# Kernel optimization log

Hardware: AMD Instinct MI355X
Metric: run time of the kernel (lower is better)

## Reference

```python
import jax, jax.numpy as jnp
import numpy as np

# dims
B, S, A = 16384, 300, 30
EMB, M_TOK, M_PROTO = 256, 8, 16
H_ENC, H_DEC, MF, NZ = 256, 128, 12, 4
ALPHA_MIN, ALPHA_MAX, ETA0 = 0.06, 0.3, 0.1
TECH_IDX = jnp.array([61, 91, 121, 151, 181, 211, 241, 271])


def setup_inputs() -> dict:
    key = jax.random.key(0)
    ks = jax.random.split(key, 20)
    def w(k, shape, fan):
        return jax.random.normal(k, shape, jnp.float32) * (fan ** -0.5)
    return {
        'state':   jax.random.uniform(ks[0], (B, S), jnp.float32),
        'fitness': jax.random.uniform(ks[1], (B, M_PROTO), jnp.float32),
        'proto_keys': jax.random.normal(ks[2], (M_PROTO, EMB), jnp.float32) * (EMB ** -0.5),
        'enc_W1': w(ks[3], (S, H_ENC), S),   'enc_b1': jnp.zeros((H_ENC,), jnp.float32),
        'ln_g':   jnp.ones((H_ENC,), jnp.float32), 'ln_b': jnp.zeros((H_ENC,), jnp.float32),
        'enc_W2': w(ks[4], (H_ENC, M_TOK * EMB), H_ENC), 'enc_b2': jnp.zeros((M_TOK * EMB,), jnp.float32),
        'dec_W1': w(ks[5], (M_PROTO, EMB, H_DEC), EMB),  'dec_b1': jnp.zeros((M_PROTO, H_DEC), jnp.float32),
        'dec_W2': w(ks[6], (M_PROTO, H_DEC, A), H_DEC),  'dec_b2': jnp.zeros((M_PROTO, A), jnp.float32),
        'tc_W':  w(ks[7], (MF, EMB), MF),  'tc_b':  jnp.zeros((EMB,), jnp.float32),
        'tc_cW': w(ks[8], (EMB, 1), EMB),  'tc_cb': jnp.zeros((1,), jnp.float32),
        'tc_zW': w(ks[9], (EMB, NZ), EMB), 'tc_zb': jnp.zeros((NZ,), jnp.float32),
        'w_prev': jnp.full((1, M_PROTO), 1.0 / M_PROTO, jnp.float32),
    }


def _layernorm(x, g, b, eps=1e-5):
    mu = x.mean(-1, keepdims=True)
    var = ((x - mu) ** 2).mean(-1, keepdims=True)
    return (x - mu) * jax.lax.rsqrt(var + eps) * g + b


def _forward(state, fitness, proto_keys, enc_W1, enc_b1, ln_g, ln_b, enc_W2, enc_b2,
             dec_W1, dec_b1, dec_W2, dec_b2, tc_W, tc_b, tc_cW, tc_cb, tc_zW, tc_zb, w_prev):
    # --- market feature extraction ---
    balance = state[:, 0:1]
    prices = state[:, 1:31]
    shares = state[:, 31:61]
    price_mean = prices.mean(1, keepdims=True)
    price_std = jnp.std(prices, axis=1, keepdims=True, ddof=1) + 1e-8  # torch.std is unbiased
    total_value = balance + (prices * shares).sum(1, keepdims=True)
    cash_ratio = balance / (total_value + 1e-8)
    tech = state[:, TECH_IDX]
    mf = jnp.concatenate([balance, price_mean, price_std, cash_ratio, tech], axis=1)  # [B,12]
    # --- T-Cell (minimal surrogate: danger embed, crisis level, crisis types) ---
    danger = jnp.tanh(mf @ tc_W + tc_b)                     # [B,EMB]
    crisis = jax.nn.sigmoid(danger @ tc_cW + tc_cb)         # [B,1]
    z = jax.nn.softmax(danger @ tc_zW + tc_zb, axis=-1)     # [B,NZ]
    # --- epitope encoder: Linear -> LN -> ReLU -> Linear -> reshape [B,m,EMB] ---
    h = jax.nn.relu(_layernorm(state @ enc_W1 + enc_b1, ln_g, ln_b))
    E = (h @ enc_W2 + enc_b2).reshape(-1, M_TOK, EMB)
    # --- IRT routing (OT-attention + fitness replicator, crisis-gated mix) ---
    scale = EMB ** -0.5
    logits = jnp.einsum('bme,ne->bmn', E, proto_keys) * scale \
           + (jnp.einsum('be,ne->bn', danger, proto_keys) * scale)[:, None, :]  # [B,m,M]
    P = jax.nn.softmax(logits, axis=-1)
    w_ot = P.mean(axis=1)                                   # [B,M]
    w_rep = w_prev * jnp.exp(ETA0 * fitness)
    w_rep = w_rep / (w_rep.sum(-1, keepdims=True) + 1e-8)
    alpha_c = ALPHA_MIN + (ALPHA_MAX - ALPHA_MIN) * (1.0 - crisis)  # [B,1]
    w = alpha_c * w_ot + (1.0 - alpha_c) * w_rep
    w = w / (w.sum(-1, keepdims=True) + 1e-8)
    # --- per-expert decoders on proto_keys (batched GEMM over M experts) ---
    hd = jax.nn.relu(jnp.einsum('me,meh->mh', proto_keys, dec_W1) + dec_b1)
    conc = jax.nn.softplus(jnp.einsum('mh,mha->ma', hd, dec_W2) + dec_b2)  # [M,A]
    mixed = jnp.einsum('bm,ma->ba', w, conc) + 1.0          # [B,A]
    # deterministic branch: softmax action head
    action = jax.nn.softmax(mixed, axis=-1)
    action = jnp.clip(action, 0.0, 1.0)
    action = action / (action.sum(-1, keepdims=True) + 1e-8)
    return action


def reference(state, fitness, proto_keys, enc_W1, enc_b1, ln_g, ln_b, enc_W2, enc_b2,
              dec_W1, dec_b1, dec_W2, dec_b2, tc_W, tc_b, tc_cW, tc_cb, tc_zW, tc_zb, w_prev):
    return _forward(state, fitness, proto_keys, enc_W1, enc_b1, ln_g, ln_b, enc_W2, enc_b2,
                    dec_W1, dec_b1, dec_W2, dec_b2, tc_W, tc_b, tc_cW, tc_cb, tc_zW, tc_zb, w_prev)
```

## Files before the change

kernel.cpp:

```cpp
#include <hip/hip_runtime.h>

typedef __attribute__((ext_vector_type(8))) short bf16x8;
typedef __attribute__((ext_vector_type(4))) float f32x4;

#define NBATCH 16384
#define SS     300
#define AA     30
#define ROWS   16
#define SSTR   352
#define HSTR   280
#define LSTR   132
#define K1P    320
#define SCALEF 0.0625f
#define ETA0   0.1f

__device__ __forceinline__ short f2b(float x) {
    unsigned u = __float_as_uint(x);
    unsigned r = (u + 0x7FFFu + ((u >> 16) & 1u)) >> 16;
    return (short)r;
}
__device__ __forceinline__ float b2f(short s) {
    return __uint_as_float(((unsigned)(unsigned short)s) << 16);
}
__device__ __forceinline__ float tanh_fast(float x) {
    float e = __expf(2.f * x);
    return 1.f - 2.f / (e + 1.f);
}

__global__ __launch_bounds__(256) void pre_kernel(
    const float* __restrict__ proto, const float* __restrict__ W1,
    const float* __restrict__ W2,   const float* __restrict__ b2,
    const float* __restrict__ tcW,  const float* __restrict__ cW,
    const float* __restrict__ dW1,  const float* __restrict__ db1,
    const float* __restrict__ dW2,  const float* __restrict__ db2,
    short* __restrict__ W1P, short* __restrict__ W3P,
    short* __restrict__ PDP, short* __restrict__ TCP,
    float* __restrict__ cmn, float* __restrict__ conc)
{
    __shared__ short sbuf[64 * 264 + 4096];
    const int t = threadIdx.x;
    const int bid = blockIdx.x;

    if (bid < 32) {
        const int m = bid >> 2, jt = bid & 3;
        short* W2s = sbuf;
        short* prS = sbuf + 64 * 264;
        #pragma unroll 4
        for (int it = 0; it < 64; ++it) {
            const int idx = it * 256 + t, j = idx >> 8, e = idx & 255;
            W2s[j * 264 + e] = f2b(W2[(size_t)(jt * 64 + j) * 2048 + m * 256 + e]);
        }
        for (int it = 0; it < 16; ++it) {
            const int id = it * 256 + t, chunk = id >> 3, j8 = id & 7;
            const int kt = chunk >> 6, rem = chunk & 63, q = rem >> 4, n = rem & 15;
            prS[id] = f2b(proto[n * 256 + kt * 32 + q * 8 + j8]);
        }
        __syncthreads();
        const int lane = t & 63, wv = t >> 6, l15 = lane & 15, q = lane >> 4;
        f32x4 acc = {0.f, 0.f, 0.f, 0.f};
        for (int kt = 0; kt < 8; ++kt) {
            bf16x8 a = *(const bf16x8*)&W2s[(wv * 16 + l15) * 264 + kt * 32 + q * 8];
            bf16x8 b = *(const bf16x8*)&prS[((kt * 4 + q) * 16 + l15) * 8];
            acc = __builtin_amdgcn_mfma_f32_16x16x32_bf16(a, b, acc, 0, 0, 0);
        }
        #pragma unroll
        for (int reg = 0; reg < 4; ++reg) {
            const int jg = jt * 64 + wv * 16 + q * 4 + reg;
            const int c = m * 16 + l15;
            const int ktj = jg >> 5, qj = (jg >> 3) & 3, j8 = jg & 7;
            W3P[((ktj * 4 + qj) * 128 + c) * 8 + j8] = f2b(acc[reg]);
        }
    } else if (bid < 42) {
        const int kt = bid - 32;
        short* W1s = sbuf;
        #pragma unroll 4
        for (int it = 0; it < 32; ++it) {
            const int idx = it * 256 + t, k = idx >> 8, n = idx & 255;
            const int kg = kt * 32 + k;
            W1s[k * 256 + n] = (kg < SS) ? f2b(W1[(size_t)kg * 256 + n]) : (short)0;
        }
        __syncthreads();
        for (int it = 0; it < 4; ++it) {
            const int id = it * 256 + t, q = id >> 8, n = id & 255;
            bf16x8 v;
            #pragma unroll
            for (int j = 0; j < 8; ++j) v[j] = W1s[(q * 8 + j) * 256 + n];
            *(bf16x8*)&W1P[((kt * 4 + q) * 256 + n) * 8] = v;
        }
    } else if (bid == 42) {
        for (int it = 0; it < 32; ++it) {
            const int id = it * 256 + t, chunk = id >> 3, j8 = id & 7;
            const int kt = chunk >> 7, q = (chunk >> 5) & 3, np = chunk & 31;
            const int k = kt * 32 + q * 8 + j8;
            float v = 0.f;
            if (np < 16) v = proto[np * 256 + k];
            else if (np == 16) v = cW[k];
            PDP[id] = f2b(v);
        }
    } else if (bid == 43) {
        for (int it = 0; it < 32; ++it) {
            const int id = it * 256 + t, chunk = id >> 3, j8 = id & 7;
            const int q = chunk >> 8, n = chunk & 255, k = q * 8 + j8;
            TCP[id] = (k < 12) ? f2b(tcW[k * 256 + n]) : (short)0;
        }
    } else if (bid == 44) {
        float* b2s = (float*)sbuf;
        float* prF = (float*)sbuf + 2048;
        for (int it = 0; it < 8; ++it)  b2s[it * 256 + t] = b2[it * 256 + t];
        for (int it = 0; it < 16; ++it) prF[it * 256 + t] = proto[it * 256 + t];
        __syncthreads();
        if (t < 128) {
            const int mq = t >> 4, n = t & 15;
            float acc = 0.f;
            for (int e = 0; e < 256; ++e) acc += b2s[mq * 256 + e] * prF[n * 256 + e];
            cmn[t] = acc;
        }
    } else {
        const int m = bid - 45;
        float* hd = (float*)sbuf;
        if (t < 128) {
            float acc = db1[m * 128 + t];
            const float* wp = dW1 + (size_t)m * 256 * 128 + t;
            const float* p = proto + m * 256;
            for (int e = 0; e < 256; ++e) acc += p[e] * wp[e * 128];
            hd[t] = fmaxf(acc, 0.f);
        }
        __syncthreads();
        if (t < AA) {
            float acc = db2[m * AA + t];
            const float* wp = dW2 + (size_t)m * 128 * AA + t;
            for (int h = 0; h < 128; ++h) acc += hd[h] * wp[h * AA];
            conc[m * AA + t] = fmaxf(acc, 0.f) + log1pf(__expf(-fabsf(acc)));
        }
    }
}

__global__ __launch_bounds__(256, 5) void main_kernel(
    const float* __restrict__ state, const float* __restrict__ fitness,
    const float* __restrict__ b1,
    const float* __restrict__ lng,  const float* __restrict__ lnb,
    const float* __restrict__ tcb,  const float* __restrict__ cb,
    const float* __restrict__ pw,
    const short* __restrict__ W1P,  const short* __restrict__ W3P,
    const short* __restrict__ PDP,  const short* __restrict__ TCP,
    const float* __restrict__ cmn,  const float* __restrict__ conc,
    float* __restrict__ out)
{
    const int t    = threadIdx.x;
    const int row0 = blockIdx.x * ROWS;
    const int w    = t >> 6;
    const int lane = t & 63;
    const int l15  = lane & 15;
    const int q    = lane >> 4;

    __shared__ short sA[ROWS * SSTR];
    __shared__ short sB[ROWS * HSTR];
    __shared__ short s_mfB[ROWS * 32];
    __shared__ float s_red[ROWS][8];
    __shared__ float s_mu[ROWS], s_rstd[ROWS];
    __shared__ float s_dd[ROWS * 16];
    __shared__ float s_crisis[ROWS];
    __shared__ float s_cmn[128];
    __shared__ float s_conc[16 * AA];

    float* s_log  = (float*)sB;
    float* s_wrep = (float*)&sA[ROWS * HSTR];

    #pragma unroll 4
    for (int it = 0; it < 20; ++it) {
        const int idx = it * 256 + t, r = idx / K1P, k = idx - r * K1P;
        sA[r * SSTR + k] = (k < SS) ? f2b(state[(size_t)(row0 + r) * SS + k]) : (short)0;
    }
    for (int it = t; it < 128 + 16 * AA; it += 256) {
        if (it < 128) s_cmn[it] = cmn[it];
        else s_conc[it - 128] = conc[it - 128];
    }
    __syncthreads();

    {
        const int r = t >> 4, g = t & 15;
        float sp = 0.f, sp2 = 0.f, sps = 0.f;
        if (g < 15) {
            #pragma unroll
            for (int jj = 0; jj < 2; ++jj) {
                const int i = 2 * g + jj;
                const float p = b2f(sA[r * SSTR + 1 + i]);
                const float s = b2f(sA[r * SSTR + 31 + i]);
                sp += p; sp2 += p * p; sps += p * s;
            }
        }
        #pragma unroll
        for (int off = 1; off < 16; off <<= 1) {
            sp  += __shfl_xor(sp, off);
            sp2 += __shfl_xor(sp2, off);
            sps += __shfl_xor(sps, off);
        }
        if (g < 8) s_mfB[r * 32 + 4 + g] = sA[r * SSTR + 61 + 30 * g];
        for (int k = 12 + g; k < 32; k += 16) s_mfB[r * 32 + k] = 0;
        if (g == 0) {
            const float bal = b2f(sA[r * SSTR]);
            const float pm = sp * (1.f / 30.f);
            const float var = (sp2 - 30.f * pm * pm) * (1.f / 29.f);
            const float pstd = sqrtf(fmaxf(var, 0.f)) + 1e-8f;
            s_mfB[r * 32 + 0] = sA[r * SSTR];
            s_mfB[r * 32 + 1] = f2b(pm);
            s_mfB[r * 32 + 2] = f2b(pstd);
            s_mfB[r * 32 + 3] = f2b(bal / (bal + sps + 1e-8f));
        }
    }
    __syncthreads();

    {
        f32x4 dacc[4];
        #pragma unroll
        for (int u = 0; u < 4; ++u) dacc[u] = (f32x4){0.f, 0.f, 0.f, 0.f};
        bf16x8 a = *(const bf16x8*)&s_mfB[l15 * 32 + q * 8];
        #pragma unroll
        for (int u = 0; u < 4; ++u) {
            bf16x8 b = *(const bf16x8*)&TCP[((q << 8) | (w * 64 + u * 16 + l15)) * 8];
            dacc[u] = __builtin_amdgcn_mfma_f32_16x16x32_bf16(a, b, dacc[u], 0, 0, 0);
        }
        #pragma unroll
        for (int u = 0; u < 4; ++u) {
            const int col = w * 64 + u * 16 + l15;
            const float tb = tcb[col];
            #pragma unroll
            for (int reg = 0; reg < 4; ++reg)
                sB[(q * 4 + reg) * HSTR + col] = f2b(tanh_fast(dacc[u][reg] + tb));
        }
    }
    __syncthreads();

    if (w == 0) {
        f32x4 acc = {0.f, 0.f, 0.f, 0.f};
        for (int kt = 0; kt < 8; ++kt) {
            bf16x8 a = *(const bf16x8*)&sB[l15 * HSTR + kt * 32 + q * 8];
            bf16x8 b = *(const bf16x8*)&PDP[((kt * 4 + q) * 32 + l15) * 8];
            acc = __builtin_amdgcn_mfma_f32_16x16x32_bf16(a, b, acc, 0, 0, 0);
        }
        #pragma unroll
        for (int reg = 0; reg < 4; ++reg)
            s_dd[(q * 4 + reg) * 16 + l15] = acc[reg];
    } else if (w == 1) {
        f32x4 acc = {0.f, 0.f, 0.f, 0.f};
        for (int kt = 0; kt < 8; ++kt) {
            bf16x8 a = *(const bf16x8*)&sB[l15 * HSTR + kt * 32 + q * 8];
            bf16x8 b = *(const bf16x8*)&PDP[((kt * 4 + q) * 32 + 16 + l15) * 8];
            acc = __builtin_amdgcn_mfma_f32_16x16x32_bf16(a, b, acc, 0, 0, 0);
        }
        if (l15 == 0) {
            const float cbv = cb[0];
            #pragma unroll
            for (int reg = 0; reg < 4; ++reg)
                s_crisis[q * 4 + reg] = 1.f / (1.f + __expf(-(acc[reg] + cbv)));
        }
    }

    f32x4 acc[4];
    #pragma unroll
    for (int u = 0; u < 4; ++u) acc[u] = (f32x4){0.f, 0.f, 0.f, 0.f};
    for (int kt = 0; kt < 10; ++kt) {
        bf16x8 a = *(const bf16x8*)&sA[l15 * SSTR + kt * 32 + q * 8];
        bf16x8 bfr[4];
        #pragma unroll
        for (int u = 0; u < 4; ++u)
            bfr[u] = *(const bf16x8*)&W1P[((kt * 4 + q) * 256 + (w * 64 + u * 16 + l15)) * 8];
        #pragma unroll
        for (int u = 0; u < 4; ++u)
            acc[u] = __builtin_amdgcn_mfma_f32_16x16x32_bf16(a, bfr[u], acc[u], 0, 0, 0);
    }

    {
        float b1v[4];
        #pragma unroll
        for (int u = 0; u < 4; ++u) b1v[u] = b1[w * 64 + u * 16 + l15];
        #pragma unroll
        for (int reg = 0; reg < 4; ++reg) {
            float s = 0.f, s2 = 0.f;
            #pragma unroll
            for (int u = 0; u < 4; ++u) {
                const float v = acc[u][reg] + b1v[u];
                acc[u][reg] = v;
                s += v; s2 += v * v;
            }
            #pragma unroll
            for (int off = 1; off < 16; off <<= 1) {
                s  += __shfl_xor(s, off);
                s2 += __shfl_xor(s2, off);
            }
            if (l15 == 0) {
                const int row = q * 4 + reg;
                s_red[row][w * 2]     = s;
                s_red[row][w * 2 + 1] = s2;
            }
        }
    }
    __syncthreads();
    if (t < ROWS) {
        float S = 0.f, S2 = 0.f;
        #pragma unroll
        for (int ww = 0; ww < 4; ++ww) { S += s_red[t][2 * ww]; S2 += s_red[t][2 * ww + 1]; }
        const float mu = S * (1.f / 256.f);
        const float var = S2 * (1.f / 256.f) - mu * mu;
        s_mu[t] = mu; s_rstd[t] = rsqrtf(var + 1e-5f);
    }
    __syncthreads();

    {
        float gv[4], bv[4];
        #pragma unroll
        for (int u = 0; u < 4; ++u) {
            gv[u] = lng[w * 64 + u * 16 + l15];
            bv[u] = lnb[w * 64 + u * 16 + l15];
        }
        #pragma unroll
        for (int reg = 0; reg < 4; ++reg) {
            const int row = q * 4 + reg;
            const float mu = s_mu[row], rs = s_rstd[row];
            #pragma unroll
            for (int u = 0; u < 4; ++u) {
                const int col = w * 64 + u * 16 + l15;
                const float v = fmaxf((acc[u][reg] - mu) * rs * gv[u] + bv[u], 0.f);
                sA[row * HSTR + col] = f2b(v);
            }
        }
    }
    __syncthreads();

    {
        f32x4 c2[2];
        c2[0] = (f32x4){0.f, 0.f, 0.f, 0.f};
        c2[1] = (f32x4){0.f, 0.f, 0.f, 0.f};
        for (int kt = 0; kt < 8; ++kt) {
            bf16x8 a = *(const bf16x8*)&sA[l15 * HSTR + kt * 32 + q * 8];
            bf16x8 b0 = *(const bf16x8*)&W3P[((kt * 4 + q) * 128 + w * 32 + l15) * 8];
            bf16x8 b1f = *(const bf16x8*)&W3P[((kt * 4 + q) * 128 + w * 32 + 16 + l15) * 8];
            c2[0] = __builtin_amdgcn_mfma_f32_16x16x32_bf16(a, b0, c2[0], 0, 0, 0);
            c2[1] = __builtin_amdgcn_mfma_f32_16x16x32_bf16(a, b1f, c2[1], 0, 0, 0);
        }
        const float cm0 = s_cmn[w * 32 + l15], cm1 = s_cmn[w * 32 + 16 + l15];
        #pragma unroll
        for (int reg = 0; reg < 4; ++reg) {
            const int row = q * 4 + reg;
            const float dd = s_dd[row * 16 + l15];
            s_log[row * LSTR + w * 32 + l15]      = SCALEF * (c2[0][reg] + cm0 + dd);
            s_log[row * LSTR + w * 32 + 16 + l15] = SCALEF * (c2[1][reg] + cm1 + dd);
        }
    }
    __syncthreads();

    if (t < 128) {
        const int r = t >> 3, m = t & 7;
        float* lg = &s_log[r * LSTR + m * 16];
        float mx = lg[0];
        #pragma unroll
        for (int n = 1; n < 16; ++n) mx = fmaxf(mx, lg[n]);
        float sum = 0.f, p[16];
        #pragma unroll
        for (int n = 0; n < 16; ++n) { p[n] = __expf(lg[n] - mx); sum += p[n]; }
        const float inv = 1.f / sum;
        #pragma unroll
        for (int n = 0; n < 16; ++n) lg[n] = p[n] * inv;
    }
    __syncthreads();

    {
        const int r = t >> 4, n = t & 15;
        float wot = 0.f;
        #pragma unroll
        for (int m = 0; m < 8; ++m) wot += s_log[r * LSTR + m * 16 + n];
        s_dd[t] = wot * 0.125f;
        s_wrep[t] = pw[n] * __expf(ETA0 * fitness[(size_t)(row0 + r) * 16 + n]);
    }
    __syncthreads();

    if (t < ROWS) {
        float srep = 0.f;
        #pragma unroll
        for (int n = 0; n < 16; ++n) srep += s_wrep[t * 16 + n];
        const float irep = 1.f / (srep + 1e-8f);
        const float alpha = 0.06f + 0.24f * (1.f - s_crisis[t]);
        float wn[16], sw = 0.f;
        #pragma unroll
        for (int n = 0; n < 16; ++n) {
            wn[n] = alpha * s_dd[t * 16 + n] + (1.f - alpha) * s_wrep[t * 16 + n] * irep;
            sw += wn[n];
        }
        const float isw = 1.f / (sw + 1e-8f);
        #pragma unroll
        for (int n = 0; n < 16; ++n) s_dd[t * 16 + n] = wn[n] * isw;
    }
    __syncthreads();

    {
        const int r = w * 4 + q;
        const int a0 = l15;
        const int a1 = a0 + 16;
        const bool v1 = a1 < AA;
        float wreg[16];
        #pragma unroll
        for (int n = 0; n < 16; ++n) wreg[n] = s_dd[r * 16 + n];
        float m0 = 1.f, m1 = 1.f;
        const int a1s = v1 ? a1 : 0;
        #pragma unroll
        for (int n = 0; n < 16; ++n) {
            m0 = fmaf(wreg[n], s_conc[n * AA + a0], m0);
            m1 = fmaf(wreg[n], s_conc[n * AA + a1s], m1);
        }
        float mx = v1 ? fmaxf(m0, m1) : m0;
        #pragma unroll
        for (int off = 1; off < 16; off <<= 1) mx = fmaxf(mx, __shfl_xor(mx, off));
        float e0 = __expf(m0 - mx);
        float e1 = v1 ? __expf(m1 - mx) : 0.f;
        float se = e0 + e1;
        #pragma unroll
        for (int off = 1; off < 16; off <<= 1) se += __shfl_xor(se, off);
        const float inv = 1.f / se;
        out[(size_t)(row0 + r) * AA + a0] = e0 * inv;
        if (v1) out[(size_t)(row0 + r) * AA + a1] = e1 * inv;
    }
}

extern "C" void kernel_launch(void* const* d_in, const int* in_sizes, int n_in,
                              void* d_out, int out_size, void* d_ws, size_t ws_size,
                              hipStream_t stream) {
    const float* state   = (const float*)d_in[0];
    const float* fitness = (const float*)d_in[1];
    const float* proto   = (const float*)d_in[2];
    const float* enc_W1  = (const float*)d_in[3];
    const float* enc_b1  = (const float*)d_in[4];
    const float* ln_g    = (const float*)d_in[5];
    const float* ln_b    = (const float*)d_in[6];
    const float* enc_W2  = (const float*)d_in[7];
    const float* enc_b2  = (const float*)d_in[8];
    const float* dec_W1  = (const float*)d_in[9];
    const float* dec_b1  = (const float*)d_in[10];
    const float* dec_W2  = (const float*)d_in[11];
    const float* dec_b2  = (const float*)d_in[12];
    const float* tc_W    = (const float*)d_in[13];
    const float* tc_b    = (const float*)d_in[14];
    const float* tc_cW   = (const float*)d_in[15];
    const float* tc_cb   = (const float*)d_in[16];
    const float* w_prev  = (const float*)d_in[19];
    float* out = (float*)d_out;

    short* W1P = (short*)d_ws;
    short* W3P = W1P + 81920;
    short* PDP = W3P + 32768;
    short* TCP = PDP + 8192;
    float* cmn  = (float*)(TCP + 8192);
    float* conc = cmn + 128;

    pre_kernel<<<61, 256, 0, stream>>>(proto, enc_W1, enc_W2, enc_b2,
                                       tc_W, tc_cW,
                                       dec_W1, dec_b1, dec_W2, dec_b2,
                                       W1P, W3P, PDP, TCP, cmn, conc);
    main_kernel<<<NBATCH / ROWS, 256, 0, stream>>>(state, fitness,
                                                   enc_b1, ln_g, ln_b,
                                                   tc_b, tc_cb, w_prev,
                                                   W1P, W3P, PDP, TCP, cmn, conc, out);
}
```

Before: 133.6 us.

## Cut barriers, vectorize state loads, and rebalance weight-prep kernel

The main kernel now loads state with float4 reads and a smaller padded stride. LayerNorm statistics are computed redundantly per thread instead of by a serial 16-thread step, which drops two barriers. The softmax over prototypes and the weight mixing are replaced by wave shuffle reductions, removing two more barriers and the serial per-row loops. The prep kernel is split across more blocks, reads proto directly, and drops an LDS transpose for W1. Redundant LDS reads and extra shuffles are added in exchange.

Result: slower. 147.0 us (+10.0%).

```diff
diff --git a/kernel.cpp b/kernel.cpp
--- a/kernel.cpp
+++ b/kernel.cpp
@@ -7,7 +7,7 @@
 #define SS     300
 #define AA     30
 #define ROWS   16
-#define SSTR   352
+#define SSTR   328
 #define HSTR   280
 #define LSTR   132
 #define K1P    320
@@ -30,98 +30,98 @@
 __global__ __launch_bounds__(256) void pre_kernel(
     const float* __restrict__ proto, const float* __restrict__ W1,
     const float* __restrict__ W2,   const float* __restrict__ b2,
-    const float* __restrict__ tcW,  const float* __restrict__ cW,
+    const float* __restrict__ tcW,  const float* __restrict__ cWp,
     const float* __restrict__ dW1,  const float* __restrict__ db1,
     const float* __restrict__ dW2,  const float* __restrict__ db2,
     short* __restrict__ W1P, short* __restrict__ W3P,
     short* __restrict__ PDP, short* __restrict__ TCP,
     float* __restrict__ cmn, float* __restrict__ conc)
 {
-    __shared__ short sbuf[64 * 264 + 4096];
+    __shared__ __align__(16) char smem[24832];
     const int t = threadIdx.x;
     const int bid = blockIdx.x;
 
-    if (bid < 32) {
-        const int m = bid >> 2, jt = bid & 3;
-        short* W2s = sbuf;
-        short* prS = sbuf + 64 * 264;
+    if (bid < 64) {
+        const int m = bid >> 3, jt = bid & 7;
+        short* W2s = (short*)smem;
+        #pragma unroll 8
+        for (int j = 0; j < 32; ++j)
+            W2s[j * 264 + t] = f2b(W2[(size_t)(jt * 32 + j) * 2048 + m * 256 + t]);
+        __syncthreads();
+        const int w = t >> 6, lane = t & 63, l15 = lane & 15, q = lane >> 4;
+        if (w < 2) {
+            f32x4 acc = {0.f, 0.f, 0.f, 0.f};
+            #pragma unroll
+            for (int kt = 0; kt < 8; ++kt) {
+                bf16x8 a = *(const bf16x8*)&W2s[(w * 16 + l15) * 264 + kt * 32 + q * 8];
+                const float4 p0 = *(const float4*)&proto[l15 * 256 + kt * 32 + q * 8];
+                const float4 p1 = *(const float4*)&proto[l15 * 256 + kt * 32 + q * 8 + 4];
+                bf16x8 b;
+                b[0] = f2b(p0.x); b[1] = f2b(p0.y); b[2] = f2b(p0.z); b[3] = f2b(p0.w);
+                b[4] = f2b(p1.x); b[5] = f2b(p1.y); b[6] = f2b(p1.z); b[7] = f2b(p1.w);
+                acc = __builtin_amdgcn_mfma_f32_16x16x32_bf16(a, b, acc, 0, 0, 0);
+            }
+            const int c = m * 16 + l15;
+            #pragma unroll
+            for (int reg = 0; reg < 4; ++reg) {
+                const int jg = jt * 32 + w * 16 + q * 4 + reg;
+                W3P[(((jg >> 5) * 4 + ((jg >> 3) & 3)) * 128 + c) * 8 + (jg & 7)] = f2b(acc[reg]);
+            }
+        }
+    } else if (bid < 74) {
+        const int kt = bid - 64;
+        const int n = t;
+        #pragma unroll
+        for (int q = 0; q < 4; ++q) {
+            bf16x8 v;
+            #pragma unroll
+            for (int j = 0; j < 8; ++j) {
+                const int kg = kt * 32 + q * 8 + j;
+                v[j] = (kg < SS) ? f2b(W1[(size_t)kg * 256 + n]) : (short)0;
+            }
+            *(bf16x8*)&W1P[((kt * 4 + q) * 256 + n) * 8] = v;
+        }
+    } else if (bid == 74) {
         #pragma unroll 4
-        for (int it = 0; it < 64; ++it) {
-            const int idx = it * 256 + t, j = idx >> 8, e = idx & 255;
-            W2s[j * 264 + e] = f2b(W2[(size_t)(jt * 64 + j) * 2048 + m * 256 + e]);
-        }
-        for (int it = 0; it < 16; ++it) {
-            const int id = it * 256 + t, chunk = id >> 3, j8 = id & 7;
-            const int kt = chunk >> 6, rem = chunk & 63, q = rem >> 4, n = rem & 15;
-            prS[id] = f2b(proto[n * 256 + kt * 32 + q * 8 + j8]);
-        }
-        __syncthreads();
-        const int lane = t & 63, wv = t >> 6, l15 = lane & 15, q = lane >> 4;
-        f32x4 acc = {0.f, 0.f, 0.f, 0.f};
-        for (int kt = 0; kt < 8; ++kt) {
-            bf16x8 a = *(const bf16x8*)&W2s[(wv * 16 + l15) * 264 + kt * 32 + q * 8];
-            bf16x8 b = *(const bf16x8*)&prS[((kt * 4 + q) * 16 + l15) * 8];
-            acc = __builtin_amdgcn_mfma_f32_16x16x32_bf16(a, b, acc, 0, 0, 0);
-        }
-        #pragma unroll
-        for (int reg = 0; reg < 4; ++reg) {
-            const int jg = jt * 64 + wv * 16 + q * 4 + reg;
-            const int c = m * 16 + l15;
-            const int ktj = jg >> 5, qj = (jg >> 3) & 3, j8 = jg & 7;
-            W3P[((ktj * 4 + qj) * 128 + c) * 8 + j8] = f2b(acc[reg]);
-        }
-    } else if (bid < 42) {
-        const int kt = bid - 32;
-        short* W1s = sbuf;
-        #pragma unroll 4
-        for (int it = 0; it < 32; ++it) {
-            const int idx = it * 256 + t, k = idx >> 8, n = idx & 255;
-            const int kg = kt * 32 + k;
-            W1s[k * 256 + n] = (kg < SS) ? f2b(W1[(size_t)kg * 256 + n]) : (short)0;
-        }
-        __syncthreads();
-        for (int it = 0; it < 4; ++it) {
-            const int id = it * 256 + t, q = id >> 8, n = id & 255;
-            bf16x8 v;
-            #pragma unroll
-            for (int j = 0; j < 8; ++j) v[j] = W1s[(q * 8 + j) * 256 + n];
-            *(bf16x8*)&W1P[((kt * 4 + q) * 256 + n) * 8] = v;
-        }
-    } else if (bid == 42) {
         for (int it = 0; it < 32; ++it) {
             const int id = it * 256 + t, chunk = id >> 3, j8 = id & 7;
             const int kt = chunk >> 7, q = (chunk >> 5) & 3, np = chunk & 31;
             const int k = kt * 32 + q * 8 + j8;
             float v = 0.f;
             if (np < 16) v = proto[np * 256 + k];
-            else if (np == 16) v = cW[k];
+            else if (np == 16) v = cWp[k];
             PDP[id] = f2b(v);
         }
-    } else if (bid == 43) {
+    } else if (bid == 75) {
+        #pragma unroll 4
         for (int it = 0; it < 32; ++it) {
             const int id = it * 256 + t, chunk = id >> 3, j8 = id & 7;
             const int q = chunk >> 8, n = chunk & 255, k = q * 8 + j8;
             TCP[id] = (k < 12) ? f2b(tcW[k * 256 + n]) : (short)0;
         }
-    } else if (bid == 44) {
-        float* b2s = (float*)sbuf;
-        float* prF = (float*)sbuf + 2048;
+    } else if (bid == 76) {
+        float* b2s = (float*)smem;
+        float* prF = b2s + 2048;
+        #pragma unroll
         for (int it = 0; it < 8; ++it)  b2s[it * 256 + t] = b2[it * 256 + t];
+        #pragma unroll
         for (int it = 0; it < 16; ++it) prF[it * 256 + t] = proto[it * 256 + t];
         __syncthreads();
         if (t < 128) {
             const int mq = t >> 4, n = t & 15;
             float acc = 0.f;
+            #pragma unroll 4
             for (int e = 0; e < 256; ++e) acc += b2s[mq * 256 + e] * prF[n * 256 + e];
             cmn[t] = acc;
         }
     } else {
-        const int m = bid - 45;
-        float* hd = (float*)sbuf;
+        const int m = bid - 77;
+        float* hd = (float*)smem;
         if (t < 128) {
             float acc = db1[m * 128 + t];
             const float* wp = dW1 + (size_t)m * 256 * 128 + t;
             const float* p = proto + m * 256;
+            #pragma unroll 4
             for (int e = 0; e < 256; ++e) acc += p[e] * wp[e * 128];
             hd[t] = fmaxf(acc, 0.f);
         }
@@ -129,6 +129,7 @@
         if (t < AA) {
             float acc = db2[m * AA + t];
             const float* wp = dW2 + (size_t)m * 128 * AA + t;
+            #pragma unroll 4
             for (int h = 0; h < 128; ++h) acc += hd[h] * wp[h * AA];
             conc[m * AA + t] = fmaxf(acc, 0.f) + log1pf(__expf(-fabsf(acc)));
         }
@@ -157,19 +158,27 @@
     __shared__ short sB[ROWS * HSTR];
     __shared__ short s_mfB[ROWS * 32];
     __shared__ float s_red[ROWS][8];
-    __shared__ float s_mu[ROWS], s_rstd[ROWS];
     __shared__ float s_dd[ROWS * 16];
     __shared__ float s_crisis[ROWS];
     __shared__ float s_cmn[128];
     __shared__ float s_conc[16 * AA];
 
-    float* s_log  = (float*)sB;
-    float* s_wrep = (float*)&sA[ROWS * HSTR];
-
-    #pragma unroll 4
-    for (int it = 0; it < 20; ++it) {
-        const int idx = it * 256 + t, r = idx / K1P, k = idx - r * K1P;
-        sA[r * SSTR + k] = (k < SS) ? f2b(state[(size_t)(row0 + r) * SS + k]) : (short)0;
+    float* s_log = (float*)sB;
+
+    #pragma unroll
+    for (int it = 0; it < 5; ++it) {
+        const int idx = it * 256 + t;
+        if (idx < ROWS * 75) {
+            const int r = idx / 75, c4 = idx - r * 75;
+            const float4 v = *(const float4*)&state[(size_t)(row0 + r) * SS + c4 * 4];
+            short4 s4;
+            s4.x = f2b(v.x); s4.y = f2b(v.y); s4.z = f2b(v.z); s4.w = f2b(v.w);
+            *(short4*)&sA[r * SSTR + c4 * 4] = s4;
+        }
+    }
+    for (int i = t; i < ROWS * 20; i += 256) {
+        const int r = i / 20, k = SS + i - r * 20;
+        sA[r * SSTR + k] = 0;
     }
     for (int it = t; it < 128 + 16 * AA; it += 256) {
         if (it < 128) s_cmn[it] = cmn[it];
@@ -270,6 +279,7 @@
             acc[u] = __builtin_amdgcn_mfma_f32_16x16x32_bf16(a, bfr[u], acc[u], 0, 0, 0);
     }
 
+    float muv[4], rsv[4];
     {
         float b1v[4];
         #pragma unroll
@@ -294,17 +304,18 @@
                 s_red[row][w * 2 + 1] = s2;
             }
         }
-    }
-    __syncthreads();
-    if (t < ROWS) {
-        float S = 0.f, S2 = 0.f;
-        #pragma unroll
-        for (int ww = 0; ww < 4; ++ww) { S += s_red[t][2 * ww]; S2 += s_red[t][2 * ww + 1]; }
-        const float mu = S * (1.f / 256.f);
-        const float var = S2 * (1.f / 256.f) - mu * mu;
-        s_mu[t] = mu; s_rstd[t] = rsqrtf(var + 1e-5f);
-    }
-    __syncthreads();
+        __syncthreads();
+        #pragma unroll
+        for (int reg = 0; reg < 4; ++reg) {
+            const int row = q * 4 + reg;
+            float S = 0.f, S2 = 0.f;
+            #pragma unroll
+            for (int ww = 0; ww < 4; ++ww) { S += s_red[row][2 * ww]; S2 += s_red[row][2 * ww + 1]; }
+            const float mu = S * (1.f / 256.f);
+            const float var = S2 * (1.f / 256.f) - mu * mu;
+            muv[reg] = mu; rsv[reg] = rsqrtf(var + 1e-5f);
+        }
+    }
 
     {
         float gv[4], bv[4];
@@ -316,11 +327,10 @@
         #pragma unroll
         for (int reg = 0; reg < 4; ++reg) {
             const int row = q * 4 + reg;
-            const float mu = s_mu[row], rs = s_rstd[row];
             #pragma unroll
             for (int u = 0; u < 4; ++u) {
                 const int col = w * 64 + u * 16 + l15;
-                const float v = fmaxf((acc[u][reg] - mu) * rs * gv[u] + bv[u], 0.f);
+                const float v = fmaxf((acc[u][reg] - muv[reg]) * rsv[reg] * gv[u] + bv[u], 0.f);
                 sA[row * HSTR + col] = f2b(v);
             }
         }
@@ -349,46 +359,34 @@
     }
     __syncthreads();
 
-    if (t < 128) {
-        const int r = t >> 3, m = t & 7;
-        float* lg = &s_log[r * LSTR + m * 16];
-        float mx = lg[0];
-        #pragma unroll
-        for (int n = 1; n < 16; ++n) mx = fmaxf(mx, lg[n]);
-        float sum = 0.f, p[16];
-        #pragma unroll
-        for (int n = 0; n < 16; ++n) { p[n] = __expf(lg[n] - mx); sum += p[n]; }
-        const float inv = 1.f / sum;
-        #pragma unroll
-        for (int n = 0; n < 16; ++n) lg[n] = p[n] * inv;
-    }
-    __syncthreads();
-
     {
         const int r = t >> 4, n = t & 15;
+        float lg[8];
+        #pragma unroll
+        for (int m = 0; m < 8; ++m) lg[m] = s_log[r * LSTR + m * 16 + n];
         float wot = 0.f;
         #pragma unroll
-        for (int m = 0; m < 8; ++m) wot += s_log[r * LSTR + m * 16 + n];
-        s_dd[t] = wot * 0.125f;
-        s_wrep[t] = pw[n] * __expf(ETA0 * fitness[(size_t)(row0 + r) * 16 + n]);
-    }
-    __syncthreads();
-
-    if (t < ROWS) {
-        float srep = 0.f;
-        #pragma unroll
-        for (int n = 0; n < 16; ++n) srep += s_wrep[t * 16 + n];
-        const float irep = 1.f / (srep + 1e-8f);
-        const float alpha = 0.06f + 0.24f * (1.f - s_crisis[t]);
-        float wn[16], sw = 0.f;
-        #pragma unroll
-        for (int n = 0; n < 16; ++n) {
-            wn[n] = alpha * s_dd[t * 16 + n] + (1.f - alpha) * s_wrep[t * 16 + n] * irep;
-            sw += wn[n];
-        }
-        const float isw = 1.f / (sw + 1e-8f);
-        #pragma unroll
-        for (int n = 0; n < 16; ++n) s_dd[t * 16 + n] = wn[n] * isw;
+        for (int m = 0; m < 8; ++m) {
+            float mx = lg[m];
+            #pragma unroll
+            for (int off = 1; off < 16; off <<= 1) mx = fmaxf(mx, __shfl_xor(mx, off));
+            const float e = __expf(lg[m] - mx);
+            float sm = e;
+            #pragma unroll
+            for (int off = 1; off < 16; off <<= 1) sm += __shfl_xor(sm, off);
+            wot += e / sm;
+        }
+        wot *= 0.125f;
+        const float wrep = pw[n] * __expf(ETA0 * fitness[(size_t)(row0 + r) * 16 + n]);
+        float srep = wrep;
+        #pragma unroll
+        for (int off = 1; off < 16; off <<= 1) srep += __shfl_xor(srep, off);
+        const float alpha = 0.06f + 0.24f * (1.f - s_crisis[r]);
+        const float wn = alpha * wot + (1.f - alpha) * wrep / (srep + 1e-8f);
+        float sw = wn;
+        #pragma unroll
+        for (int off = 1; off < 16; off <<= 1) sw += __shfl_xor(sw, off);
+        s_dd[t] = wn / (sw + 1e-8f);
     }
     __syncthreads();
 
@@ -451,7 +449,7 @@
     float* cmn  = (float*)(TCP + 8192);
     float* conc = cmn + 128;
 
-    pre_kernel<<<61, 256, 0, stream>>>(proto, enc_W1, enc_W2, enc_b2,
+    pre_kernel<<<93, 256, 0, stream>>>(proto, enc_W1, enc_W2, enc_b2,
                                        tc_W, tc_cW,
                                        dec_W1, dec_b1, dec_W2, dec_b2,
                                        W1P, W3P, PDP, TCP, cmn, conc);
```
